# Optimization experiments

Measured on AMD Instinct MI355X. Metric: run time of the kernel, lower is better.

Reference implementation:

```python
import jax, jax.numpy as jnp
import numpy as np
import math

B, S, D_IN, D_OUT, H = 2, 2048, 1024, 1024, 16
HD = D_OUT // H


def setup_inputs() -> dict:
    key = jax.random.key(0)
    ks = jax.random.split(key, 6)
    scale = 0.02
    return {
        "x": jax.random.normal(ks[0], (B, S, D_IN), dtype=jnp.float32),
        "Wq": jax.random.normal(ks[1], (D_IN, D_OUT), dtype=jnp.float32) * scale,
        "Wk": jax.random.normal(ks[2], (D_IN, D_OUT), dtype=jnp.float32) * scale,
        "Wv": jax.random.normal(ks[3], (D_IN, D_OUT), dtype=jnp.float32) * scale,
        "Wo": jax.random.normal(ks[4], (D_OUT, D_OUT), dtype=jnp.float32) * scale,
        "bo": jax.random.normal(ks[5], (D_OUT,), dtype=jnp.float32) * scale,
    }


def reference(x, Wq, Wk, Wv, Wo, bo):
    b, n, _ = x.shape
    # project and split heads -> [b, h, n, hd]
    q = (x @ Wq).reshape(b, n, H, HD).transpose(0, 2, 1, 3)
    k = (x @ Wk).reshape(b, n, H, HD).transpose(0, 2, 1, 3)
    v = (x @ Wv).reshape(b, n, H, HD).transpose(0, 2, 1, 3)
    # materialized [b, h, n, n] scores with causal mask (as in original)
    scores = jnp.einsum('bhqd,bhkd->bhqk', q, k)
    causal = jnp.tril(jnp.ones((n, n), dtype=bool))  # True = keep
    scores = jnp.where(causal, scores, -jnp.inf)
    attn = jax.nn.softmax(scores / math.sqrt(HD), axis=-1)
    ctx = jnp.einsum('bhqk,bhkd->bhqd', attn, v)
    ctx = ctx.transpose(0, 2, 1, 3).reshape(b, n, D_OUT)
    return ctx @ Wo + bo
```

## Files before the change

### kernel.cpp

```cpp
#include <hip/hip_runtime.h>
#include <hip/hip_bf16.h>
#include <math.h>

typedef __bf16 v8bf __attribute__((ext_vector_type(8)));
typedef __bf16 v4bf __attribute__((ext_vector_type(4)));
typedef short  v4s  __attribute__((ext_vector_type(4)));
typedef float  v4f  __attribute__((ext_vector_type(4)));
typedef unsigned short u16;

static_assert(sizeof(v8bf) == 16, "v8bf must be 16B");

__device__ __forceinline__ u16 f2bf(float f) {
  __hip_bfloat16 h = __float2bfloat16(f);
  return *reinterpret_cast<u16*>(&h);
}
__device__ __forceinline__ v4f mfma16(v8bf a, v8bf b, v4f c) {
  return __builtin_amdgcn_mfma_f32_16x16x32_bf16(a, b, c, 0, 0, 0);
}
__device__ __forceinline__ v4f mfma16k16(v4bf a, v4bf b, v4f c) {
#if __has_builtin(__builtin_amdgcn_mfma_f32_16x16x16_bf16)
  return __builtin_amdgcn_mfma_f32_16x16x16_bf16(a, b, c, 0, 0, 0);
#else
  union { v4bf f; v4s s; } ua, ub;
  ua.f = a; ub.f = b;
  return __builtin_amdgcn_mfma_f32_16x16x16bf16_1k(ua.s, ub.s, c, 0, 0, 0);
#endif
}
__device__ __forceinline__ void async16(const u16* g, u16* l) {
  __builtin_amdgcn_global_load_lds(
      (__attribute__((address_space(1))) void*)(void*)g,
      (__attribute__((address_space(3))) void*)l, 16, 0, 0);
}

__global__ void prep(const float* __restrict__ x, const float* __restrict__ Wq,
                     const float* __restrict__ Wk, const float* __restrict__ Wv,
                     const float* __restrict__ Wo, u16* __restrict__ Wt,
                     u16* __restrict__ xb) {
  int tx = threadIdx.x, ty = threadIdx.y;
  if (blockIdx.z == 4) {
    int bid = blockIdx.y * 32 + blockIdx.x;
    int i = (bid * 1024 + ty * 32 + tx) * 4;
    float4 v = *(const float4*)(x + i);
    ushort4 o;
    o.x = f2bf(v.x); o.y = f2bf(v.y); o.z = f2bf(v.z); o.w = f2bf(v.w);
    *(ushort4*)(xb + i) = o;
    return;
  }
  __shared__ float tile[32][33];
  const float* src = (blockIdx.z == 0) ? Wq : (blockIdx.z == 1) ? Wk : (blockIdx.z == 2) ? Wv : Wo;
  int k0 = blockIdx.x * 32, n0 = blockIdx.y * 32;
  tile[ty][tx] = src[(size_t)(k0 + ty) * 1024 + n0 + tx];
  __syncthreads();
  Wt[(size_t)(blockIdx.z * 1024 + n0 + ty) * 1024 + k0 + tx] = f2bf(tile[tx][ty]);
}

__global__ __launch_bounds__(512) void gemm_qkv(const u16* __restrict__ xb,
                                                const u16* __restrict__ Wt,
                                                u16* __restrict__ Qb,
                                                u16* __restrict__ Kb,
                                                u16* __restrict__ Vt) {
  extern __shared__ __align__(16) u16 lds[];
  u16* sA = lds;
  u16* sB = lds + 32768;

  const int t = threadIdx.x;
  const int w = t >> 6, l = t & 63;
  const int quad = l >> 4, low = l & 15;
  const int wm = (w & 1) * 128, wn = (w >> 1) * 64;
  const int bm = blockIdx.x, bn = blockIdx.y;

  const int srow = l >> 3;
  const int cg = (l & 7) ^ srow;

  auto SA_ = [&](int R0, int kb, u16* dst) {
    async16(xb + (size_t)(bm * 256 + R0 + w * 8 + srow) * 1024 + kb + cg * 8,
            dst + (R0 + w * 8) * 64);
  };
  auto SB_ = [&](int R0, int kb, u16* dst) {
    async16(Wt + (size_t)(bn * 256 + R0 + w * 8 + srow) * 1024 + kb + cg * 8,
            dst + (R0 + w * 8) * 64);
  };

  v4f acc[8][4] = {};

  SB_(0, 0, sB); SB_(64, 0, sB); SB_(128, 0, sB); SB_(192, 0, sB);
  SA_(0, 0, sA); SA_(128, 0, sA); SA_(64, 0, sA); SA_(192, 0, sA);

#pragma unroll 2
  for (int kt = 0; kt < 16; ++kt) {
    const int p = kt & 1;
    const u16* pa = sA + p * 16384;
    const u16* pb = sB + p * 16384;
    u16* nA = sA + (p ^ 1) * 16384;
    u16* nB = sB + (p ^ 1) * 16384;
    const int nkb = (kt + 1) * 64;
    const bool more = (kt < 15);

    asm volatile("s_waitcnt lgkmcnt(0)" ::: "memory");
    asm volatile("s_waitcnt vmcnt(2)" ::: "memory");
    __builtin_amdgcn_s_barrier();

    v8bf bf[2][4];
#pragma unroll
    for (int j = 0; j < 4; j++) {
      const int rb = wn + j * 16 + low, sw = rb & 7;
      bf[0][j] = *(const v8bf*)(pb + rb * 64 + ((quad ^ sw) * 8));
      bf[1][j] = *(const v8bf*)(pb + rb * 64 + (((4 + quad) ^ sw) * 8));
    }
#pragma unroll
    for (int ph = 0; ph < 4; ++ph) {
      if (ph == 2) {
        if (more) asm volatile("s_waitcnt vmcnt(4)" ::: "memory");
        else      asm volatile("s_waitcnt vmcnt(0)" ::: "memory");
        __builtin_amdgcn_s_barrier();
      }
      v8bf a0k0, a0k1, a1k0, a1k1;
      {
        const int ra = wm + (2 * ph) * 16 + low, sw = ra & 7;
        a0k0 = *(const v8bf*)(pa + ra * 64 + ((quad ^ sw) * 8));
        a0k1 = *(const v8bf*)(pa + ra * 64 + (((4 + quad) ^ sw) * 8));
      }
      {
        const int ra = wm + (2 * ph + 1) * 16 + low, sw = ra & 7;
        a1k0 = *(const v8bf*)(pa + ra * 64 + ((quad ^ sw) * 8));
        a1k1 = *(const v8bf*)(pa + ra * 64 + (((4 + quad) ^ sw) * 8));
      }
      if (more) {
        if (ph == 0)      { SB_(0, nkb, nB);   SB_(64, nkb, nB); }
        else if (ph == 1) { SB_(128, nkb, nB); SB_(192, nkb, nB); }
        else if (ph == 2) { SA_(0, nkb, nA);   SA_(128, nkb, nA); }
        else              { SA_(64, nkb, nA);  SA_(192, nkb, nA); }
      }
      __builtin_amdgcn_s_setprio(1);
#pragma unroll
      for (int j = 0; j < 4; j++) {
        acc[2 * ph][j]     = mfma16(a0k0, bf[0][j], acc[2 * ph][j]);
        acc[2 * ph][j]     = mfma16(a0k1, bf[1][j], acc[2 * ph][j]);
        acc[2 * ph + 1][j] = mfma16(a1k0, bf[0][j], acc[2 * ph + 1][j]);
        acc[2 * ph + 1][j] = mfma16(a1k1, bf[1][j], acc[2 * ph + 1][j]);
      }
      __builtin_amdgcn_s_setprio(0);
    }
  }

  const int zone = bn >> 2;
  const float qsc = (zone == 0) ? 0.18033688011112042f : 1.0f;
#pragma unroll
  for (int i = 0; i < 8; i++) {
    int m0 = bm * 256 + wm + i * 16 + quad * 4;
#pragma unroll
    for (int j = 0; j < 4; j++) {
      int nn = (bn * 256 + wn + j * 16 + low) & 1023;
      if (zone == 0) {
#pragma unroll
        for (int r = 0; r < 4; r++)
          Qb[(size_t)(m0 + r) * 1024 + nn] = f2bf(acc[i][j][r] * qsc);
      } else if (zone == 1) {
#pragma unroll
        for (int r = 0; r < 4; r++)
          Kb[(size_t)(m0 + r) * 1024 + nn] = f2bf(acc[i][j][r]);
      } else {
        int bb = m0 >> 11, s = m0 & 2047;
#pragma unroll
        for (int r = 0; r < 4; r++)
          Vt[(size_t)(bb * 1024 + nn) * 2048 + s + r] = f2bf(acc[i][j][r]);
      }
    }
  }
}

__global__ __launch_bounds__(256) void gemm_out(const u16* __restrict__ ctx,
                                                const u16* __restrict__ Wt,
                                                const float* __restrict__ bo,
                                                float* __restrict__ out) {
  __shared__ __align__(16) u16 sA[128 * 32];
  __shared__ __align__(16) u16 sB[64 * 32];
  const u16* Bt = Wt + (size_t)3072 * 1024;
  v4f acc[4][2] = {};
  const int bm = blockIdx.x, bn = blockIdx.y;
  const int t = threadIdx.x, w = t >> 6, l = t & 63, quad = l >> 4, low = l & 15;
  const int wm = (w & 1) * 64, wn = (w >> 1) * 32;
  const int rowA = bm * 128 + w * 32 + (l >> 2);
  const int rowB = bn * 64 + w * 16 + (l >> 2);
  const int col8 = (l & 3) * 8;
  u16* la = sA + w * 1024;
  u16* lb = sB + w * 512;

  for (int kb = 0; kb < 1024; kb += 32) {
    async16(ctx + (size_t)rowA * 1024 + kb + col8, la);
    async16(ctx + (size_t)(rowA + 16) * 1024 + kb + col8, la + 512);
    async16(Bt + (size_t)rowB * 1024 + kb + col8, lb);
    __syncthreads();
    v8bf af[4], bfr[2];
#pragma unroll
    for (int i = 0; i < 4; i++)
      af[i] = *(const v8bf*)(sA + (wm + i * 16 + low) * 32 + quad * 8);
#pragma unroll
    for (int j = 0; j < 2; j++)
      bfr[j] = *(const v8bf*)(sB + (wn + j * 16 + low) * 32 + quad * 8);
#pragma unroll
    for (int i = 0; i < 4; i++)
#pragma unroll
      for (int j = 0; j < 2; j++)
        acc[i][j] = mfma16(af[i], bfr[j], acc[i][j]);
    __syncthreads();
  }
#pragma unroll
  for (int i = 0; i < 4; i++) {
    int m0 = bm * 128 + wm + i * 16 + quad * 4;
#pragma unroll
    for (int j = 0; j < 2; j++) {
      int n = bn * 64 + wn + j * 16 + low;
      float bias = bo[n];
#pragma unroll
      for (int r = 0; r < 4; r++)
        out[(size_t)(m0 + r) * 1024 + n] = acc[i][j][r] + bias;
    }
  }
}

__global__ __launch_bounds__(256) void attn(const u16* __restrict__ Qb,
                                            const u16* __restrict__ Kb,
                                            const u16* __restrict__ Vt,
                                            u16* __restrict__ ctx) {
  __shared__ __align__(16) u16 sK[4][4096];
  __shared__ __align__(16) u16 sV[4][4096];
  const int t = threadIdx.x, w = t >> 6, l = t & 63, quad = l >> 4, low = l & 15;

  const int bid = blockIdx.x;
  const int xcd = bid & 7, slot = bid >> 3;
  const int pair = xcd * 4 + (slot & 3);
  const int tp = slot >> 2;
  const int b = pair >> 4, h = pair & 15;

  const u16* kbase = Kb + (size_t)(b * 2048) * 1024 + h * 64;
  const u16* vbase = Vt + (size_t)(b * 1024 + h * 64) * 2048;

  const int srow = l >> 3;
  const int cg = (l & 7) ^ srow;

  auto STAGE = [&](int tt, int bi) {
    const int kb = tt * 64;
    const u16* kg = kbase + (size_t)(kb + w * 8 + srow) * 1024 + cg * 8;
    async16(kg, &sK[bi][w * 512]);
    async16(kg + (size_t)32 * 1024, &sK[bi][2048 + w * 512]);
    const u16* vg = vbase + (size_t)(w * 8 + srow) * 2048 + kb + cg * 8;
    async16(vg, &sV[bi][w * 512]);
    async16(vg + (size_t)32 * 2048, &sV[bi][2048 + w * 512]);
  };

  for (int ph = 0; ph < 2; ++ph) {
    const int tile = ph ? tp : 31 - tp;
    const int nkt = tile + 1;
    const int qw = tile * 64 + w * 16;

    if (ph) {
      asm volatile("s_waitcnt lgkmcnt(0)" ::: "memory");
      __builtin_amdgcn_s_barrier();
    }

    const u16* qrow_p = Qb + (size_t)(b * 2048 + qw + low) * 1024 + h * 64;
    v8bf qa0 = *(const v8bf*)(qrow_p + quad * 8);
    v8bf qa1 = *(const v8bf*)(qrow_p + 32 + quad * 8);
    asm volatile("" ::: "memory");

    float li = 0.f;
    v4f o[4] = {};

    STAGE(0, 0);
    if (nkt > 1) STAGE(1, 1);

    for (int it = 0; it < nkt; ++it) {
      const int bi = it & 3;
      if (it + 2 < nkt) STAGE(it + 2, (it + 2) & 3);
      asm volatile("s_waitcnt lgkmcnt(0)" ::: "memory");
      const int c = nkt - 1 - it;
      if (c >= 2)      asm volatile("s_waitcnt vmcnt(8)" ::: "memory");
      else if (c == 1) asm volatile("s_waitcnt vmcnt(4)" ::: "memory");
      else             asm volatile("s_waitcnt vmcnt(0)" ::: "memory");
      __builtin_amdgcn_s_barrier();

      const int kb = it * 64;
      v4f s[4] = {};
      __builtin_amdgcn_s_setprio(1);
#pragma unroll
      for (int cf = 0; cf < 4; cf++) {
        const int key = cf * 16 + low;
        v8bf kf0 = *(const v8bf*)(&sK[bi][key * 64 + ((quad ^ (key & 7)) * 8)]);
        v8bf kf1 = *(const v8bf*)(&sK[bi][key * 64 + (((4 + quad) ^ (key & 7)) * 8)]);
        s[cf] = mfma16(kf0, qa0, s[cf]);
        s[cf] = mfma16(kf1, qa1, s[cf]);
      }
      __builtin_amdgcn_s_setprio(0);

      const bool dm = (it == nkt - 1);
      const int qr = qw + low;
      v4bf pf[4];
#pragma unroll
      for (int cf = 0; cf < 4; cf++)
#pragma unroll
        for (int r = 0; r < 4; r++) {
          float e = __builtin_amdgcn_exp2f(s[cf][r]);
          if (dm && (kb + cf * 16 + quad * 4 + r > qr)) e = 0.f;
          li += e;
          pf[cf][r] = (__bf16)e;
        }

      __builtin_amdgcn_s_setprio(1);
#pragma unroll
      for (int df = 0; df < 4; df++) {
        const int d = df * 16 + low;
#pragma unroll
        for (int cf = 0; cf < 4; cf++) {
          const int c2 = cf * 2 + (quad >> 1);
          const v4bf vf = *(const v4bf*)(&sV[bi][d * 64 + ((c2 ^ (d & 7)) * 8) + (quad & 1) * 4]);
          o[df] = mfma16k16(pf[cf], vf, o[df]);
        }
      }
      __builtin_amdgcn_s_setprio(0);
    }

    li += __shfl_xor(li, 16);
    li += __shfl_xor(li, 32);

#pragma unroll
    for (int r = 0; r < 4; r++) {
      float lir = __shfl(li, quad * 4 + r);
      float inv = 1.f / lir;
      int row = b * 2048 + qw + quad * 4 + r;
#pragma unroll
      for (int df = 0; df < 4; df++)
        ctx[(size_t)row * 1024 + h * 64 + df * 16 + low] = f2bf(o[df][r] * inv);
    }
  }
}

extern "C" void kernel_launch(void* const* d_in, const int* in_sizes, int n_in,
                              void* d_out, int out_size, void* d_ws, size_t ws_size,
                              hipStream_t stream) {
  const float* x  = (const float*)d_in[0];
  const float* Wq = (const float*)d_in[1];
  const float* Wk = (const float*)d_in[2];
  const float* Wv = (const float*)d_in[3];
  const float* Wo = (const float*)d_in[4];
  const float* bo = (const float*)d_in[5];
  float* out = (float*)d_out;

  char* ws = (char*)d_ws;
  u16* xb  = (u16*)(ws);
  u16* Wt  = (u16*)(ws + 8ull * 1024 * 1024);
  u16* Qb  = (u16*)(ws + 16ull * 1024 * 1024);
  u16* Kb  = (u16*)(ws + 24ull * 1024 * 1024);
  u16* Vt  = (u16*)(ws + 32ull * 1024 * 1024);
  u16* ctx = (u16*)(ws + 40ull * 1024 * 1024);

  static bool cfg = false;
  if (!cfg) {
    hipFuncSetAttribute((const void*)gemm_qkv,
                        hipFuncAttributeMaxDynamicSharedMemorySize, 131072);
    cfg = true;
  }

  prep<<<dim3(32, 32, 5), dim3(32, 32, 1), 0, stream>>>(x, Wq, Wk, Wv, Wo, Wt, xb);
  gemm_qkv<<<dim3(16, 12, 1), dim3(512, 1, 1), 131072, stream>>>(xb, Wt, Qb, Kb, Vt);
  attn<<<dim3(512, 1, 1), dim3(256, 1, 1), 0, stream>>>(Qb, Kb, Vt, ctx);
  gemm_out<<<dim3(32, 16, 1), dim3(256, 1, 1), 0, stream>>>(ctx, Wt, bo, out);
}
```

Before: 175.7 us.

## Process two query tiles per block sharing K/V tiles in attention

```diff
diff --git a/kernel.cpp b/kernel.cpp
--- a/kernel.cpp
+++ b/kernel.cpp
@@ -223,15 +223,12 @@
                                             const u16* __restrict__ Kb,
                                             const u16* __restrict__ Vt,
                                             u16* __restrict__ ctx) {
-  __shared__ __align__(16) u16 sK[4][4096];
-  __shared__ __align__(16) u16 sV[4][4096];
+  __shared__ __align__(16) u16 sK[2][4096];
+  __shared__ __align__(16) u16 sV[2][4096];
   const int t = threadIdx.x, w = t >> 6, l = t & 63, quad = l >> 4, low = l & 15;
-
-  const int bid = blockIdx.x;
-  const int xcd = bid & 7, slot = bid >> 3;
-  const int pair = xcd * 4 + (slot & 3);
-  const int tp = slot >> 2;
-  const int b = pair >> 4, h = pair & 15;
+  const int h = blockIdx.x, tile = 15 - blockIdx.y, b = blockIdx.z;
+  const int qw0 = tile * 128 + w * 16, qw1 = qw0 + 64;
+  const int nkt = 2 * (tile + 1);
 
   const u16* kbase = Kb + (size_t)(b * 2048) * 1024 + h * 64;
   const u16* vbase = Vt + (size_t)(b * 1024 + h * 64) * 2048;
@@ -239,98 +236,99 @@
   const int srow = l >> 3;
   const int cg = (l & 7) ^ srow;
 
-  auto STAGE = [&](int tt, int bi) {
-    const int kb = tt * 64;
-    const u16* kg = kbase + (size_t)(kb + w * 8 + srow) * 1024 + cg * 8;
-    async16(kg, &sK[bi][w * 512]);
-    async16(kg + (size_t)32 * 1024, &sK[bi][2048 + w * 512]);
-    const u16* vg = vbase + (size_t)(w * 8 + srow) * 2048 + kb + cg * 8;
-    async16(vg, &sV[bi][w * 512]);
-    async16(vg + (size_t)32 * 2048, &sV[bi][2048 + w * 512]);
-  };
-
-  for (int ph = 0; ph < 2; ++ph) {
-    const int tile = ph ? tp : 31 - tp;
-    const int nkt = tile + 1;
-    const int qw = tile * 64 + w * 16;
-
-    if (ph) {
-      asm volatile("s_waitcnt lgkmcnt(0)" ::: "memory");
-      __builtin_amdgcn_s_barrier();
-    }
-
-    const u16* qrow_p = Qb + (size_t)(b * 2048 + qw + low) * 1024 + h * 64;
-    v8bf qa0 = *(const v8bf*)(qrow_p + quad * 8);
-    v8bf qa1 = *(const v8bf*)(qrow_p + 32 + quad * 8);
-    asm volatile("" ::: "memory");
-
-    float li = 0.f;
-    v4f o[4] = {};
-
-    STAGE(0, 0);
-    if (nkt > 1) STAGE(1, 1);
-
-    for (int it = 0; it < nkt; ++it) {
-      const int bi = it & 3;
-      if (it + 2 < nkt) STAGE(it + 2, (it + 2) & 3);
-      asm volatile("s_waitcnt lgkmcnt(0)" ::: "memory");
-      const int c = nkt - 1 - it;
-      if (c >= 2)      asm volatile("s_waitcnt vmcnt(8)" ::: "memory");
-      else if (c == 1) asm volatile("s_waitcnt vmcnt(4)" ::: "memory");
-      else             asm volatile("s_waitcnt vmcnt(0)" ::: "memory");
-      __builtin_amdgcn_s_barrier();
-
-      const int kb = it * 64;
-      v4f s[4] = {};
-      __builtin_amdgcn_s_setprio(1);
+  const u16* qp0 = Qb + (size_t)(b * 2048 + qw0 + low) * 1024 + h * 64;
+  v8bf qa00 = *(const v8bf*)(qp0 + quad * 8);
+  v8bf qa01 = *(const v8bf*)(qp0 + 32 + quad * 8);
+  const u16* qp1 = Qb + (size_t)(b * 2048 + qw1 + low) * 1024 + h * 64;
+  v8bf qa10 = *(const v8bf*)(qp1 + quad * 8);
+  v8bf qa11 = *(const v8bf*)(qp1 + 32 + quad * 8);
+
+  float li0 = 0.f, li1 = 0.f;
+  v4f o0[4] = {}, o1[4] = {};
+
+  {
+    const u16* kg = kbase + (size_t)(w * 8 + srow) * 1024 + cg * 8;
+    async16(kg, &sK[0][w * 512]);
+    async16(kg + (size_t)32 * 1024, &sK[0][2048 + w * 512]);
+    const u16* vg = vbase + (size_t)(w * 8 + srow) * 2048 + cg * 8;
+    async16(vg, &sV[0][w * 512]);
+    async16(vg + (size_t)32 * 2048, &sV[0][2048 + w * 512]);
+  }
+
+  for (int it = 0; it < nkt; it++) {
+    __syncthreads();
+    const int kb = it * 64;
+    const int cur = it & 1;
+    if (it + 1 < nkt) {
+      const int nb = (it + 1) & 1;
+      const u16* kg = kbase + (size_t)(kb + 64 + w * 8 + srow) * 1024 + cg * 8;
+      async16(kg, &sK[nb][w * 512]);
+      async16(kg + (size_t)32 * 1024, &sK[nb][2048 + w * 512]);
+      const u16* vg = vbase + (size_t)(w * 8 + srow) * 2048 + kb + 64 + cg * 8;
+      async16(vg, &sV[nb][w * 512]);
+      async16(vg + (size_t)32 * 2048, &sV[nb][2048 + w * 512]);
+    }
+
+    v4f s0[4] = {}, s1[4] = {};
+#pragma unroll
+    for (int cf = 0; cf < 4; cf++) {
+      const int key = cf * 16 + low;
+      v8bf kf0 = *(const v8bf*)(&sK[cur][key * 64 + ((quad ^ (key & 7)) * 8)]);
+      v8bf kf1 = *(const v8bf*)(&sK[cur][key * 64 + (((4 + quad) ^ (key & 7)) * 8)]);
+      s0[cf] = mfma16(kf0, qa00, s0[cf]);
+      s0[cf] = mfma16(kf1, qa01, s0[cf]);
+      s1[cf] = mfma16(kf0, qa10, s1[cf]);
+      s1[cf] = mfma16(kf1, qa11, s1[cf]);
+    }
+
+    const bool dm = (it >= nkt - 2);
+    const int qr0 = qw0 + low, qr1 = qw1 + low;
+    v4bf pf0[4], pf1[4];
+#pragma unroll
+    for (int cf = 0; cf < 4; cf++)
+#pragma unroll
+      for (int r = 0; r < 4; r++) {
+        float e0 = __builtin_amdgcn_exp2f(s0[cf][r]);
+        float e1 = __builtin_amdgcn_exp2f(s1[cf][r]);
+        if (dm) {
+          const int key = kb + cf * 16 + quad * 4 + r;
+          if (key > qr0) e0 = 0.f;
+          if (key > qr1) e1 = 0.f;
+        }
+        li0 += e0; li1 += e1;
+        pf0[cf][r] = (__bf16)e0;
+        pf1[cf][r] = (__bf16)e1;
+      }
+
+#pragma unroll
+    for (int df = 0; df < 4; df++) {
+      const int d = df * 16 + low;
 #pragma unroll
       for (int cf = 0; cf < 4; cf++) {
-        const int key = cf * 16 + low;
-        v8bf kf0 = *(const v8bf*)(&sK[bi][key * 64 + ((quad ^ (key & 7)) * 8)]);
-        v8bf kf1 = *(const v8bf*)(&sK[bi][key * 64 + (((4 + quad) ^ (key & 7)) * 8)]);
-        s[cf] = mfma16(kf0, qa0, s[cf]);
-        s[cf] = mfma16(kf1, qa1, s[cf]);
-      }
-      __builtin_amdgcn_s_setprio(0);
-
-      const bool dm = (it == nkt - 1);
-      const int qr = qw + low;
-      v4bf pf[4];
-#pragma unroll
-      for (int cf = 0; cf < 4; cf++)
-#pragma unroll
-        for (int r = 0; r < 4; r++) {
-          float e = __builtin_amdgcn_exp2f(s[cf][r]);
-          if (dm && (kb + cf * 16 + quad * 4 + r > qr)) e = 0.f;
-          li += e;
-          pf[cf][r] = (__bf16)e;
-        }
-
-      __builtin_amdgcn_s_setprio(1);
-#pragma unroll
-      for (int df = 0; df < 4; df++) {
-        const int d = df * 16 + low;
-#pragma unroll
-        for (int cf = 0; cf < 4; cf++) {
-          const int c2 = cf * 2 + (quad >> 1);
-          const v4bf vf = *(const v4bf*)(&sV[bi][d * 64 + ((c2 ^ (d & 7)) * 8) + (quad & 1) * 4]);
-          o[df] = mfma16k16(pf[cf], vf, o[df]);
-        }
-      }
-      __builtin_amdgcn_s_setprio(0);
-    }
-
-    li += __shfl_xor(li, 16);
-    li += __shfl_xor(li, 32);
-
-#pragma unroll
-    for (int r = 0; r < 4; r++) {
-      float lir = __shfl(li, quad * 4 + r);
-      float inv = 1.f / lir;
-      int row = b * 2048 + qw + quad * 4 + r;
-#pragma unroll
-      for (int df = 0; df < 4; df++)
-        ctx[(size_t)row * 1024 + h * 64 + df * 16 + low] = f2bf(o[df][r] * inv);
+        const int c2 = cf * 2 + (quad >> 1);
+        const v4bf vf = *(const v4bf*)(&sV[cur][d * 64 + ((c2 ^ (d & 7)) * 8) + (quad & 1) * 4]);
+        o0[df] = mfma16k16(pf0[cf], vf, o0[df]);
+        o1[df] = mfma16k16(pf1[cf], vf, o1[df]);
+      }
+    }
+  }
+
+  li0 += __shfl_xor(li0, 16);
+  li0 += __shfl_xor(li0, 32);
+  li1 += __shfl_xor(li1, 16);
+  li1 += __shfl_xor(li1, 32);
+
+#pragma unroll
+  for (int r = 0; r < 4; r++) {
+    float l0 = __shfl(li0, quad * 4 + r);
+    float l1 = __shfl(li1, quad * 4 + r);
+    float inv0 = 1.f / l0, inv1 = 1.f / l1;
+    int row0 = b * 2048 + qw0 + quad * 4 + r;
+    int row1 = b * 2048 + qw1 + quad * 4 + r;
+#pragma unroll
+    for (int df = 0; df < 4; df++) {
+      ctx[(size_t)row0 * 1024 + h * 64 + df * 16 + low] = f2bf(o0[df][r] * inv0);
+      ctx[(size_t)row1 * 1024 + h * 64 + df * 16 + low] = f2bf(o1[df][r] * inv1);
     }
   }
 }
@@ -363,6 +361,6 @@
 
   prep<<<dim3(32, 32, 5), dim3(32, 32, 1), 0, stream>>>(x, Wq, Wk, Wv, Wo, Wt, xb);
   gemm_qkv<<<dim3(16, 12, 1), dim3(512, 1, 1), 131072, stream>>>(xb, Wt, Qb, Kb, Vt);
-  attn<<<dim3(512, 1, 1), dim3(256, 1, 1), 0, stream>>>(Qb, Kb, Vt, ctx);
+  attn<<<dim3(16, 16, 2), dim3(256, 1, 1), 0, stream>>>(Qb, Kb, Vt, ctx);
   gemm_out<<<dim3(32, 16, 1), dim3(256, 1, 1), 0, stream>>>(ctx, Wt, bo, out);
 }
```

After: 195.7 us. 1.11x slower.
